# Performance work log

Measured on AMD Instinct MI355X. Metric: run time of the kernel, lower is better.

## Reference

```python
import jax, jax.numpy as jnp
import numpy as np

E = 64       # expert_nums
D = 32       # embed_dim
H = 4        # num_heads
HD = D // H  # head_dim = 8
B = 524288
TOP_K = 2
NOISE_EPS = 0.01


def setup_inputs() -> dict:
    key = jax.random.key(0)
    ks = jax.random.split(key, 10)
    return {
        "taskID": jax.random.randint(ks[0], (B,), 0, 6),
        "embed_table": jax.random.normal(ks[1], (6, D), jnp.float32),
        "expert_keys": jax.random.normal(ks[2], (D, D), jnp.float32),
        "in_proj_w": jax.random.normal(ks[3], (3 * D, D), jnp.float32) * 0.1,
        "in_proj_b": jax.random.normal(ks[4], (3 * D,), jnp.float32) * 0.1,
        "fc_gate_w": jax.random.normal(ks[5], (E, D), jnp.float32) * 0.1,
        "fc_gate_b": jax.random.normal(ks[6], (E,), jnp.float32) * 0.1,
        "fc_noise_w": jax.random.normal(ks[7], (E, D), jnp.float32) * 0.1,
        "fc_noise_b": jax.random.normal(ks[8], (E,), jnp.float32) * 0.1,
        "noise": jax.random.normal(ks[9], (B, E), jnp.float32),
    }


def reference(taskID, embed_table, expert_keys, in_proj_w, in_proj_b,
              fc_gate_w, fc_gate_b, fc_noise_w, fc_noise_b, noise):
    bsz = taskID.shape[0]
    x = embed_table[taskID]                                   # [B, D] task embeddings (query)
    # nn.MultiheadAttention q/k projections (v and out_proj don't affect attn_weights)
    Wq, Wk = in_proj_w[:D], in_proj_w[D:2 * D]
    bq, bk = in_proj_b[:D], in_proj_b[D:2 * D]
    Q = (x @ Wq.T + bq).reshape(bsz, H, HD)                   # [B, H, HD]
    K = (expert_keys @ Wk.T + bk).reshape(D, H, HD)           # [S=32, H, HD], shared across batch
    scores = jnp.einsum('bhd,shd->bhs', Q, K) / np.sqrt(HD).astype(np.float32)
    attn_w = jax.nn.softmax(scores, axis=-1).mean(axis=1)     # averaged over heads -> [B, 32]
    expert_weight = jax.nn.softmax(attn_w, axis=-1)           # module re-applies softmax (faithful)
    clean_logits = expert_weight @ fc_gate_w.T + fc_gate_b    # [B, E]
    noise_std = jax.nn.softplus(expert_weight @ fc_noise_w.T + fc_noise_b) + NOISE_EPS
    logits = clean_logits + noise * noise_std                 # train=True path
    top_logits, top_indices = jax.lax.top_k(logits, min(TOP_K + 1, E))
    tk_logits = top_logits[:, :TOP_K]                         # [B, TOP_K]
    tk_indices = top_indices[:, :TOP_K]
    tk_gates = jax.nn.softmax(tk_logits, axis=-1)
    rows = jnp.arange(bsz)[:, None]
    gates = jnp.zeros_like(logits).at[rows, tk_indices].set(tk_gates)  # scatter sparse gates
    load = gates.sum(axis=0)                                  # [E]
    return gates, load
```

## Files before the change

### kernel.cpp

```cpp
#include <hip/hip_runtime.h>
#include <math.h>

#define NE 64
#define NTASK 6
#define BLK 256
#define GRID 1024
#define RPI 32

__global__ void precompute_kernel(
    const float* __restrict__ embed_table,
    const float* __restrict__ expert_keys,
    const float* __restrict__ in_proj_w,
    const float* __restrict__ in_proj_b,
    const float* __restrict__ fc_gate_w,
    const float* __restrict__ fc_gate_b,
    const float* __restrict__ fc_noise_w,
    const float* __restrict__ fc_noise_b,
    float*   __restrict__ tab_f,
    double2* __restrict__ tab_d,
    float*   __restrict__ load)
{
    __shared__ float s_win[96 * 32];
    __shared__ float s_wg[64 * 32];
    __shared__ float s_wn[64 * 32];
    __shared__ float s_keys[32 * 32];
    __shared__ float s_emb[6 * 32];
    __shared__ float s_bin[96], s_bg[64], s_bn[64];
    __shared__ double Ksh[32][32];
    __shared__ double Qsh[6][32];
    __shared__ double sc[24][32];
    __shared__ double attn[6][32];
    __shared__ double ew[6][32];
    __shared__ double red[24];
    __shared__ double red2[6];
    const int tid = threadIdx.x;

    if (tid < NE) load[tid] = 0.f;

    for (int i = tid; i < 96 * 32; i += BLK) s_win[i] = in_proj_w[i];
    for (int i = tid; i < 64 * 32; i += BLK) { s_wg[i] = fc_gate_w[i]; s_wn[i] = fc_noise_w[i]; }
    for (int i = tid; i < 32 * 32; i += BLK) s_keys[i] = expert_keys[i];
    for (int i = tid; i < 6 * 32;  i += BLK) s_emb[i] = embed_table[i];
    if (tid < 96) s_bin[tid] = in_proj_b[tid];
    if (tid < 64) { s_bg[tid] = fc_gate_b[tid]; s_bn[tid] = fc_noise_b[tid]; }
    __syncthreads();

    for (int idx = tid; idx < 32 * 32; idx += BLK) {
        int s = idx >> 5, j = idx & 31;
        double acc = (double)s_bin[32 + j];
        for (int d = 0; d < 32; ++d)
            acc += (double)s_keys[s * 32 + d] * (double)s_win[(32 + j) * 32 + d];
        Ksh[s][j] = acc;
    }
    for (int idx = tid; idx < NTASK * 32; idx += BLK) {
        int t = idx >> 5, j = idx & 31;
        double acc = (double)s_bin[j];
        for (int d = 0; d < 32; ++d)
            acc += (double)s_emb[t * 32 + d] * (double)s_win[j * 32 + d];
        Qsh[t][j] = acc;
    }
    __syncthreads();

    const double SCALE = 1.0 / (double)((float)2.8284271247461903);
    for (int idx = tid; idx < 24 * 32; idx += BLK) {
        int th = idx >> 5, s = idx & 31;
        int t = th >> 2, h = th & 3;
        double acc = 0.0;
        for (int d = 0; d < 8; ++d)
            acc += Qsh[t][h * 8 + d] * Ksh[s][h * 8 + d];
        sc[th][s] = acc * SCALE;
    }
    __syncthreads();
    if (tid < 24) {
        double m = sc[tid][0];
        for (int s = 1; s < 32; ++s) m = fmax(m, sc[tid][s]);
        red[tid] = m;
    }
    __syncthreads();
    for (int idx = tid; idx < 24 * 32; idx += BLK) {
        int th = idx >> 5, s = idx & 31;
        sc[th][s] = exp(sc[th][s] - red[th]);
    }
    __syncthreads();
    if (tid < 24) {
        double sum = 0.0;
        for (int s = 0; s < 32; ++s) sum += sc[tid][s];
        red[tid] = 1.0 / sum;
    }
    __syncthreads();
    for (int idx = tid; idx < NTASK * 32; idx += BLK) {
        int t = idx >> 5, s = idx & 31;
        attn[t][s] = 0.25 * (sc[t*4+0][s]*red[t*4+0] + sc[t*4+1][s]*red[t*4+1]
                           + sc[t*4+2][s]*red[t*4+2] + sc[t*4+3][s]*red[t*4+3]);
    }
    __syncthreads();
    if (tid < NTASK) {
        double m = attn[tid][0];
        for (int s = 1; s < 32; ++s) m = fmax(m, attn[tid][s]);
        red2[tid] = m;
    }
    __syncthreads();
    for (int idx = tid; idx < NTASK * 32; idx += BLK) {
        int t = idx >> 5, s = idx & 31;
        ew[t][s] = exp(attn[t][s] - red2[t]);
    }
    __syncthreads();
    if (tid < NTASK) {
        double sum = 0.0;
        for (int s = 0; s < 32; ++s) sum += ew[tid][s];
        red2[tid] = 1.0 / sum;
    }
    __syncthreads();

    {
        float2* tab_f2 = (float2*)tab_f;
        for (int idx = tid; idx < NTASK * NE; idx += BLK) {
            int t = idx >> 6, e = idx & 63;
            double inv = red2[t];
            double a  = (double)s_bg[e];
            double n0 = (double)s_bn[e];
            for (int d = 0; d < 32; ++d) {
                double w = ew[t][d] * inv;
                a  += w * (double)s_wg[e * 32 + d];
                n0 += w * (double)s_wn[e * 32 + d];
            }
            double sp = (n0 > 0.0) ? (n0 + log1p(exp(-n0))) : log1p(exp(n0));
            double ns = sp + 0.01;
            const int p  = e >> 1;
            const int cc = (p >> 3) & 3, rr = p & 7;
            const int i4 = t * 32 + p;
            const int dst = (i4 & ~7) | (rr ^ ((2 * cc + t) & 7));
            tab_f2[dst * 2 + (e & 1)] = make_float2((float)a, (float)ns);
            tab_d[t * 64 + e] = make_double2(a, ns);
        }
        for (int idx = NTASK * NE + tid; idx < 512; idx += BLK) {
            tab_f2[idx] = make_float2(0.f, 0.f);
        }
    }
}

__global__ __launch_bounds__(BLK) void router_kernel(
    const int*     __restrict__ taskID,
    const float4*  __restrict__ noise4,
    const float4*  __restrict__ tabf4,
    const double2* __restrict__ tabd,
    float4* __restrict__ gates4,
    float*  __restrict__ load,
    int B)
{
    __shared__ float4  s_tabf4[256];
    __shared__ double2 s_tabd[512];
    __shared__ float   s_load[NE];
    __shared__ float4  s_stage[BLK/64][256];

    const int tid = threadIdx.x;
    for (int i = tid; i < 256; i += BLK) s_tabf4[i] = tabf4[i];
    for (int i = tid; i < 512; i += BLK) s_tabd[i] = tabd[i];
    if (tid < NE) s_load[tid] = 0.f;
    __syncthreads();

    const int lane  = tid & 63;
    const int wid   = tid >> 6;
    const int sub   = lane >> 2;
    const int c     = lane & 3;
    const int ebase = c * 16;
    const int W = (blockIdx.x * BLK + tid) >> 6;
    const int nWaves = GRID * (BLK / 64);
    const int nGroup = (B + RPI - 1) / RPI;
    const int n4 = B * 16;
    const float4 zero4 = make_float4(0.f, 0.f, 0.f, 0.f);

    float4 cur[8], nxt[8];
    int tA = 0, tB = 0;

    {
        const int gb = W * 512;
        #pragma unroll
        for (int j = 0; j < 8; ++j) {
            const int idx = gb + j * 64 + lane;
            cur[j] = (W < nGroup && idx < n4) ? noise4[idx] : zero4;
        }
        const int rA = W * RPI + sub, rB = rA + 16;
        tA = (W < nGroup && rA < B) ? taskID[rA] : 0;
        tB = (W < nGroup && rB < B) ? taskID[rB] : 0;
    }

    for (int g = W; g < nGroup; g += nWaves) {
        const int gn = g + nWaves;
        {
            const int gb = gn * 512;
            #pragma unroll
            for (int j = 0; j < 8; ++j) {
                const int idx = gb + j * 64 + lane;
                nxt[j] = (gn < nGroup && idx < n4) ? noise4[idx] : zero4;
            }
        }
        int ntA = 0, ntB = 0;
        {
            const int rA = gn * RPI + sub, rB = rA + 16;
            ntA = (gn < nGroup && rA < B) ? taskID[rA] : 0;
            ntB = (gn < nGroup && rB < B) ? taskID[rB] : 0;
        }

#define INS2(l_, e_, n_) {                                                     \
        const bool b1_ = (l_) > v1, b2_ = (l_) > v2;                           \
        v2 = b1_ ? v1 : (b2_ ? (l_) : v2);                                     \
        i2 = b1_ ? i1 : (b2_ ? (e_) : i2);                                     \
        n2 = b1_ ? n1 : (b2_ ? (n_) : n2);                                     \
        v1 = b1_ ? (l_) : v1;                                                  \
        i1 = b1_ ? (e_) : i1;                                                  \
        n1 = b1_ ? (n_) : n1; }

#define STEP(r_, nlo_, nhi_) {                                                 \
        const float4 tv = s_tabf4[tb + ((r_) ^ x)];                            \
        const float l0 = __fadd_rn(tv.x, __fmul_rn((nlo_), tv.y));             \
        const float l1 = __fadd_rn(tv.z, __fmul_rn((nhi_), tv.w));             \
        INS2(l0, ebase + 2 * (r_),     (nlo_));                                \
        INS2(l1, ebase + 2 * (r_) + 1, (nhi_)); }

#define PROCHALF(t_, rowbase_, cj0, cj1, cj2, cj3)                             \
    {                                                                          \
                         \
        _Pragma("unroll")                                                      \
        for (int j = 0; j < 4; ++j) {                                          \
            const float4 vsrc = (j == 0) ? (cj0) : (j == 1) ? (cj1)            \
                              : (j == 2) ? (cj2) : (cj3);                      \
            const int f  = j * 64 + lane;                                      \
            const int rl = f >> 4, q = f & 15;                                 \
            s_stage[wid][rl * 16 + (q ^ rl)] = vsrc;                           \
        }                                                                      \
        float4 z[4];                                                           \
        _Pragma("unroll")                                                      \
        for (int k = 0; k < 4; ++k)                                            \
            z[k] = s_stage[wid][sub * 16 + ((c * 4 + k) ^ sub)];               \
        const int t  = (t_);                                                   \
        const int x  = (2 * c + t) & 7;                                        \
        const int tb = t * 32 + c * 8;                                         \
        float v1 = -INFINITY, v2 = -INFINITY;                                  \
        int   i1 = 0, i2 = 0;                                                  \
        float n1 = 0.f, n2 = 0.f;                                              \
        STEP(0, z[0].x, z[0].y); STEP(1, z[0].z, z[0].w);                      \
        STEP(2, z[1].x, z[1].y); STEP(3, z[1].z, z[1].w);                      \
        STEP(4, z[2].x, z[2].y); STEP(5, z[2].z, z[2].w);                      \
        STEP(6, z[3].x, z[3].y); STEP(7, z[3].z, z[3].w);                      \
        _Pragma("unroll")                                                      \
        for (int m = 1; m <= 2; m <<= 1) {                                     \
            const float w1 = __shfl_xor(v1, m), w2 = __shfl_xor(v2, m);        \
            const int   j1 = __shfl_xor(i1, m), j2 = __shfl_xor(i2, m);        \
            const float q1 = __shfl_xor(n1, m), q2 = __shfl_xor(n2, m);        \
            const bool aw = (v1 > w1) || (v1 == w1 && i1 < j1);                \
            const float p1 = aw ? v1 : w1, p2 = aw ? v2 : w2;                  \
            const int   pi1 = aw ? i1 : j1, pi2 = aw ? i2 : j2;                \
            const float pn1 = aw ? n1 : q1, pn2 = aw ? n2 : q2;                \
            const float u1 = aw ? w1 : v1;                                     \
            const int   ui1 = aw ? j1 : i1;                                    \
            const float un1 = aw ? q1 : n1;                                    \
            const bool b2 = (p2 > u1) || (p2 == u1 && pi2 < ui1);              \
            v1 = p1;  i1 = pi1; n1 = pn1;                                      \
            v2 = b2 ? p2 : u1;  i2 = b2 ? pi2 : ui1;  n2 = b2 ? pn2 : un1;     \
        }                                                                      \
        const double2 A  = s_tabd[t * 64 + i1];                                \
        const double2 Bt = s_tabd[t * 64 + i2];                                \
        double da = A.x  + (double)n1 * A.y;  int ia = i1;                     \
        double db = Bt.x + (double)n2 * Bt.y; int ib = i2;                     \
        if (db > da || (db == da && ib < ia)) {                                \
            double tv_ = da; da = db; db = tv_;                                \
            int ti_ = ia; ia = ib; ib = ti_;                                   \
        }                                                                      \
        const float e2 = expf((float)(db - da));                               \
        const float g1 = 1.0f / (1.0f + e2);                                   \
        const float g2 = e2 / (1.0f + e2);                                     \
        const int iab = ia | (ib << 8);                                        \
        if (c == 0 && ((rowbase_) + sub) < B) {                                \
            atomicAdd(&s_load[ia], g1);                                        \
            atomicAdd(&s_load[ib], g2);                                        \
        }                                                                      \
         \
        const int gb_ = (rowbase_) * 16;                                       \
        _Pragma("unroll")                                                      \
        for (int j = 0; j < 4; ++j) {                                          \
            const int f  = j * 64 + lane;                                      \
            const int rr = f >> 4;                                             \
            const int p  = f & 15;                                             \
            const int src = rr << 2;                                           \
            const int   siab = __shfl(iab, src);                               \
            const float sg1  = __shfl(g1,  src);                               \
            const float sg2  = __shfl(g2,  src);                               \
            const int sia = siab & 255, sib = siab >> 8;                       \
            const int e0 = p * 4;                                              \
            float4 w;                                                          \
            w.x = (e0 + 0 == sia) ? sg1 : ((e0 + 0 == sib) ? sg2 : 0.f);       \
            w.y = (e0 + 1 == sia) ? sg1 : ((e0 + 1 == sib) ? sg2 : 0.f);       \
            w.z = (e0 + 2 == sia) ? sg1 : ((e0 + 2 == sib) ? sg2 : 0.f);       \
            w.w = (e0 + 3 == sia) ? sg1 : ((e0 + 3 == sib) ? sg2 : 0.f);       \
            const int gidx = gb_ + f;                                          \
            if (gidx < n4) gates4[gidx] = w;                                   \
        }                                                                      \
    }

        PROCHALF(tA, g * RPI,      cur[0], cur[1], cur[2], cur[3])
        PROCHALF(tB, g * RPI + 16, cur[4], cur[5], cur[6], cur[7])

#undef PROCHALF
#undef STEP
#undef INS2

        #pragma unroll
        for (int j = 0; j < 8; ++j) cur[j] = nxt[j];
        tA = ntA; tB = ntB;
    }
    __syncthreads();
    if (tid < NE) atomicAdd(&load[tid], s_load[tid]);
}

extern "C" void kernel_launch(void* const* d_in, const int* in_sizes, int n_in,
                              void* d_out, int out_size, void* d_ws, size_t ws_size,
                              hipStream_t stream) {
    const int*   taskID      = (const int*)  d_in[0];
    const float* embed_table = (const float*)d_in[1];
    const float* expert_keys = (const float*)d_in[2];
    const float* in_proj_w   = (const float*)d_in[3];
    const float* in_proj_b   = (const float*)d_in[4];
    const float* fc_gate_w   = (const float*)d_in[5];
    const float* fc_gate_b   = (const float*)d_in[6];
    const float* fc_noise_w  = (const float*)d_in[7];
    const float* fc_noise_b  = (const float*)d_in[8];
    const float* noise       = (const float*)d_in[9];

    const int B = in_sizes[0];

    float*   tab_f = (float*)d_ws;
    double2* tab_d = (double2*)((char*)d_ws + 4096);

    float* gates = (float*)d_out;
    float* load  = gates + (size_t)B * NE;

    precompute_kernel<<<1, BLK, 0, stream>>>(embed_table, expert_keys, in_proj_w, in_proj_b,
                                             fc_gate_w, fc_gate_b, fc_noise_w, fc_noise_b,
                                             tab_f, tab_d, load);

    router_kernel<<<GRID, BLK, 0, stream>>>(taskID, (const float4*)noise,
                                            (const float4*)tab_f, tab_d,
                                            (float4*)gates, load, B);
}
```

Before: 119.6 us.

## Replace persistent grid-stride loop with one-group-per-wave launch

```diff
diff --git a/kernel.cpp b/kernel.cpp
--- a/kernel.cpp
+++ b/kernel.cpp
@@ -4,7 +4,6 @@
 #define NE 64
 #define NTASK 6
 #define BLK 256
-#define GRID 1024
 #define RPI 32
 
 __global__ void precompute_kernel(
@@ -153,54 +152,36 @@
     __shared__ float   s_load[NE];
     __shared__ float4  s_stage[BLK/64][256];
 
-    const int tid = threadIdx.x;
-    for (int i = tid; i < 256; i += BLK) s_tabf4[i] = tabf4[i];
-    for (int i = tid; i < 512; i += BLK) s_tabd[i] = tabd[i];
-    if (tid < NE) s_load[tid] = 0.f;
-    __syncthreads();
-
-    const int lane  = tid & 63;
-    const int wid   = tid >> 6;
-    const int sub   = lane >> 2;
-    const int c     = lane & 3;
+    const int tid  = threadIdx.x;
+    const int lane = tid & 63;
+    const int wid  = tid >> 6;
+    const int sub  = lane >> 2;
+    const int c    = lane & 3;
     const int ebase = c * 16;
-    const int W = (blockIdx.x * BLK + tid) >> 6;
-    const int nWaves = GRID * (BLK / 64);
+    const int W = blockIdx.x * (BLK / 64) + wid;
     const int nGroup = (B + RPI - 1) / RPI;
     const int n4 = B * 16;
     const float4 zero4 = make_float4(0.f, 0.f, 0.f, 0.f);
-
-    float4 cur[8], nxt[8];
+    const bool active = W < nGroup;
+
+    float4 cur[8];
     int tA = 0, tB = 0;
-
     {
         const int gb = W * 512;
         #pragma unroll
         for (int j = 0; j < 8; ++j) {
             const int idx = gb + j * 64 + lane;
-            cur[j] = (W < nGroup && idx < n4) ? noise4[idx] : zero4;
+            cur[j] = (active && idx < n4) ? noise4[idx] : zero4;
         }
         const int rA = W * RPI + sub, rB = rA + 16;
-        tA = (W < nGroup && rA < B) ? taskID[rA] : 0;
-        tB = (W < nGroup && rB < B) ? taskID[rB] : 0;
-    }
-
-    for (int g = W; g < nGroup; g += nWaves) {
-        const int gn = g + nWaves;
-        {
-            const int gb = gn * 512;
-            #pragma unroll
-            for (int j = 0; j < 8; ++j) {
-                const int idx = gb + j * 64 + lane;
-                nxt[j] = (gn < nGroup && idx < n4) ? noise4[idx] : zero4;
-            }
-        }
-        int ntA = 0, ntB = 0;
-        {
-            const int rA = gn * RPI + sub, rB = rA + 16;
-            ntA = (gn < nGroup && rA < B) ? taskID[rA] : 0;
-            ntB = (gn < nGroup && rB < B) ? taskID[rB] : 0;
-        }
+        tA = (active && rA < B) ? taskID[rA] : 0;
+        tB = (active && rB < B) ? taskID[rB] : 0;
+    }
+
+    for (int i = tid; i < 256; i += BLK) s_tabf4[i] = tabf4[i];
+    for (int i = tid; i < 512; i += BLK) s_tabd[i] = tabd[i];
+    if (tid < NE) s_load[tid] = 0.f;
+    __syncthreads();
 
 #define INS2(l_, e_, n_) {                                                     \
         const bool b1_ = (l_) > v1, b2_ = (l_) > v2;                           \
@@ -220,7 +201,6 @@
 
 #define PROCHALF(t_, rowbase_, cj0, cj1, cj2, cj3)                             \
     {                                                                          \
-                         \
         _Pragma("unroll")                                                      \
         for (int j = 0; j < 4; ++j) {                                          \
             const float4 vsrc = (j == 0) ? (cj0) : (j == 1) ? (cj1)            \
@@ -275,7 +255,6 @@
             atomicAdd(&s_load[ia], g1);                                        \
             atomicAdd(&s_load[ib], g2);                                        \
         }                                                                      \
-         \
         const int gb_ = (rowbase_) * 16;                                       \
         _Pragma("unroll")                                                      \
         for (int j = 0; j < 4; ++j) {                                          \
@@ -298,17 +277,15 @@
         }                                                                      \
     }
 
-        PROCHALF(tA, g * RPI,      cur[0], cur[1], cur[2], cur[3])
-        PROCHALF(tB, g * RPI + 16, cur[4], cur[5], cur[6], cur[7])
+    if (active) {
+        PROCHALF(tA, W * RPI,      cur[0], cur[1], cur[2], cur[3])
+        PROCHALF(tB, W * RPI + 16, cur[4], cur[5], cur[6], cur[7])
+    }
 
 #undef PROCHALF
 #undef STEP
 #undef INS2
 
-        #pragma unroll
-        for (int j = 0; j < 8; ++j) cur[j] = nxt[j];
-        tA = ntA; tB = ntB;
-    }
     __syncthreads();
     if (tid < NE) atomicAdd(&load[tid], s_load[tid]);
 }
@@ -339,7 +316,9 @@
                                              fc_gate_w, fc_gate_b, fc_noise_w, fc_noise_b,
                                              tab_f, tab_d, load);
 
-    router_kernel<<<GRID, BLK, 0, stream>>>(taskID, (const float4*)noise,
+    const int nGroup = (B + RPI - 1) / RPI;
+    const int grid   = (nGroup + (BLK / 64) - 1) / (BLK / 64);
+    router_kernel<<<grid, BLK, 0, stream>>>(taskID, (const float4*)noise,
                                             (const float4*)tab_f, tab_d,
                                             (float4*)gates, load, B);
 }
```

After: 167.7 us. 40.2% more time.
